# Kernel tuning notes

Hardware: AMD Instinct MI355X
Metric: run time of the kernel (lower is better)

## Reference

```python
import jax, jax.numpy as jnp
import numpy as np
from jax import lax

B, T, I, H, L = 256, 512, 156, 128, 32


def setup_inputs() -> dict:
    key = jax.random.key(0)
    ks = jax.random.split(key, 16)
    kb = 1.0 / np.sqrt(H)  # torch default LSTM/Linear init bound

    def u(k, shape, bound):
        return jax.random.uniform(k, shape, minval=-bound, maxval=bound, dtype=jnp.float32)

    return {
        "motion": jax.random.normal(ks[0], (B, T, I), dtype=jnp.float32),
        "eps": jax.random.normal(ks[1], (B, L), dtype=jnp.float32),
        # encoder LSTM (gate order i,f,g,o; b = b_ih + b_hh folded together)
        "enc_Wih": u(ks[2], (4 * H, I), kb),
        "enc_Whh": u(ks[3], (4 * H, H), kb),
        "enc_b": u(ks[4], (4 * H,), kb),
        "mu_W": u(ks[5], (L, H), kb),
        "mu_b": u(ks[6], (L,), kb),
        "var_W": u(ks[7], (L, H), kb),
        "var_b": u(ks[8], (L,), kb),
        # decoder
        "dec_fc_W": u(ks[9], (H, L), 1.0 / np.sqrt(L)),
        "dec_fc_b": u(ks[10], (H,), 1.0 / np.sqrt(L)),
        "dec_Wih": u(ks[11], (4 * H, H), kb),
        "dec_Whh": u(ks[12], (4 * H, H), kb),
        "dec_b": u(ks[13], (4 * H,), kb),
        "out_W": u(ks[14], (I, H), kb),
        "out_b": u(ks[15], (I,), kb),
    }


def _cell(gates, c):
    # PyTorch LSTM gate layout: [i, f, g, o] along the 4H axis
    i, f, g, o = jnp.split(gates, 4, axis=-1)
    c_new = jax.nn.sigmoid(f) * c + jax.nn.sigmoid(i) * jnp.tanh(g)
    h_new = jax.nn.sigmoid(o) * jnp.tanh(c_new)
    return h_new, c_new


def reference(motion, eps, enc_Wih, enc_Whh, enc_b, mu_W, mu_b, var_W, var_b,
              dec_fc_W, dec_fc_b, dec_Wih, dec_Whh, dec_b, out_W, out_b):
    b, t, _ = motion.shape

    # ---- encoder LSTM: single scan over time, keep only final hidden ----
    def enc_step(carry, x_t):
        h, c = carry
        gates = x_t @ enc_Wih.T + h @ enc_Whh.T + enc_b
        h, c = _cell(gates, c)
        return (h, c), None

    h0 = jnp.zeros((b, H), motion.dtype)
    c0 = jnp.zeros((b, H), motion.dtype)
    (h_fin, _), _ = lax.scan(enc_step, (h0, c0), jnp.swapaxes(motion, 0, 1))

    mu = h_fin @ mu_W.T + mu_b          # [B, L]
    logvar = h_fin @ var_W.T + var_b    # [B, L] ('var' in the torch code)

    # ---- reparameterize ----
    z = mu + eps * jnp.exp(0.5 * logvar)

    # ---- decoder: input at each step is the previous hidden state ----
    dh0 = z @ dec_fc_W.T + dec_fc_b     # [B, H]
    dc0 = jnp.zeros((b, H), motion.dtype)

    def dec_step(carry, _):
        h, c = carry
        gates = h @ dec_Wih.T + h @ dec_Whh.T + dec_b
        h, c = _cell(gates, c)
        return (h, c), h

    _, hs = lax.scan(dec_step, (dh0, dc0), None, length=t)  # [T, B, H]
    recon = jnp.einsum('tbh,oh->bto', hs, out_W) + out_b    # [B, T, I]

    # ---- losses ----
    rec_loss = jnp.mean((recon - motion) ** 2)
    kl_loss = -0.5 * jnp.sum(1.0 + logvar - mu ** 2 - jnp.exp(logvar))
    total = rec_loss + kl_loss
    return recon, mu, logvar, total
```

## Files before the change

### kernel.cpp

```cpp
#include <hip/hip_runtime.h>
#include <hip/hip_fp16.h>

#define B_ 256
#define T_ 512
#define I_ 156
#define H_ 128
#define L_ 32
#define G_ 512

typedef _Float16 half_t;
typedef _Float16 h2_t __attribute__((ext_vector_type(2)));

union U8 { uint4 u; h2_t h2[4]; };

__device__ __forceinline__ float fdot2(h2_t a, h2_t b, float c) {
#if __has_builtin(__builtin_amdgcn_fdot2)
  return __builtin_amdgcn_fdot2(a, b, c, false);
#else
  return c + (float)a[0] * (float)b[0] + (float)a[1] * (float)b[1];
#endif
}

__device__ __forceinline__ h2_t pk2(float a, float b) {
  h2_t r; r[0] = (half_t)a; r[1] = (half_t)b; return r;
}

__device__ __forceinline__ float sigf(float x) { return 1.0f / (1.0f + __expf(-x)); }
__device__ __forceinline__ float tanhf_(float x) {
  x = fminf(fmaxf(x, -20.f), 20.f);
  float e = __expf(2.f * x);
  return (e - 1.f) / (e + 1.f);
}

__global__ __launch_bounds__(1024, 4) void enc_kernel(
    const float* __restrict__ motion, const float* __restrict__ eps,
    const float* __restrict__ Wih, const float* __restrict__ Whh,
    const float* __restrict__ bv,
    const float* __restrict__ muW, const float* __restrict__ mub,
    const float* __restrict__ varW, const float* __restrict__ varb,
    const float* __restrict__ fcW, const float* __restrict__ fcb,
    float* __restrict__ dout, float* __restrict__ dh0,
    float* __restrict__ accums)
{
  const int tid  = threadIdx.x;
  const int part = tid >> 9;
  const int j    = tid & 511;
  const int b    = blockIdx.x;

  __shared__ h2_t xs[2][80];
  __shared__ h2_t hs[64];
  __shared__ float gl2[2][G_];
  __shared__ float hf[H_];
  __shared__ float mulv[64];
  __shared__ float zs[L_];

  h2_t wih[40];
  h2_t whh[32];
  {
    const int cbase = part * 80;
    const float* wr = Wih + (size_t)j * I_;
#pragma unroll
    for (int k = 0; k < 40; ++k) {
      int c0 = cbase + 2 * k;
      float a = (c0     < I_) ? wr[c0]     : 0.f;
      float c = (c0 + 1 < I_) ? wr[c0 + 1] : 0.f;
      wih[k] = pk2(a, c);
    }
    const float2* r2 = (const float2*)(Whh + (size_t)j * H_ + part * 64);
#pragma unroll
    for (int k = 0; k < 32; ++k) { float2 w = r2[k]; whh[k] = pk2(w.x, w.y); }
  }

  float cb0 = 0.f, cb1 = 0.f, cb2 = 0.f, cb3 = 0.f;
  if (tid < H_) {
    cb0 = bv[tid]; cb1 = bv[tid + H_]; cb2 = bv[tid + 2*H_]; cb3 = bv[tid + 3*H_];
  }

  float creg = 0.f, hreg = 0.f;
  if (tid < 64) hs[tid] = pk2(0.f, 0.f);
  if (tid < 4)  xs[tid >> 1][78 + (tid & 1)] = pk2(0.f, 0.f);

  const float2* mrow = (const float2*)(motion + (size_t)b * T_ * I_);
  const bool loader = (part == 1) && (j < 78);
  if (loader) { float2 m = mrow[j]; xs[0][j] = pk2(m.x, m.y); }
  __syncthreads();

  int cur = 0;
  float2 xreg;
  for (int t = 0; t < T_; ++t) {
    if (loader && t + 1 < T_) xreg = mrow[(t + 1) * 78 + j];

    float a0 = 0.f, a1 = 0.f, a2 = 0.f, a3 = 0.f;
    const U8* xv = (const U8*)&xs[cur][part * 40];
#pragma unroll
    for (int c = 0; c < 10; ++c) {
      U8 v = xv[c];
      a0 = fdot2(wih[4*c+0], v.h2[0], a0);
      a1 = fdot2(wih[4*c+1], v.h2[1], a1);
      a2 = fdot2(wih[4*c+2], v.h2[2], a2);
      a3 = fdot2(wih[4*c+3], v.h2[3], a3);
    }
    const U8* hv = (const U8*)&hs[part * 32];
#pragma unroll
    for (int c = 0; c < 8; ++c) {
      U8 v = hv[c];
      a0 = fdot2(whh[4*c+0], v.h2[0], a0);
      a1 = fdot2(whh[4*c+1], v.h2[1], a1);
      a2 = fdot2(whh[4*c+2], v.h2[2], a2);
      a3 = fdot2(whh[4*c+3], v.h2[3], a3);
    }
    gl2[part][j] = (a0 + a1) + (a2 + a3);
    if (loader && t + 1 < T_) xs[cur ^ 1][j] = pk2(xreg.x, xreg.y);
    __syncthreads();

    if (tid < H_) {
      float ig = gl2[0][tid]         + gl2[1][tid]         + cb0;
      float fg = gl2[0][tid +   H_]  + gl2[1][tid +   H_]  + cb1;
      float gg = gl2[0][tid + 2*H_]  + gl2[1][tid + 2*H_]  + cb2;
      float og = gl2[0][tid + 3*H_]  + gl2[1][tid + 3*H_]  + cb3;
      creg = sigf(fg) * creg + sigf(ig) * tanhf_(gg);
      hreg = sigf(og) * tanhf_(creg);
      ((half_t*)hs)[tid] = (half_t)hreg;
    }
    __syncthreads();
    cur ^= 1;
  }

  if (tid < H_) hf[tid] = hreg;
  __syncthreads();

  if (tid < 64) {
    const float* wr = (tid < L_) ? (muW + tid * H_) : (varW + (tid - L_) * H_);
    float a = (tid < L_) ? mub[tid] : varb[tid - L_];
#pragma unroll 8
    for (int k = 0; k < H_; ++k) a += wr[k] * hf[k];
    mulv[tid] = a;
    if (tid < L_) dout[(size_t)B_*T_*I_ + b * L_ + tid] = a;
    else          dout[(size_t)B_*T_*I_ + B_*L_ + b * L_ + (tid - L_)] = a;
  }
  __syncthreads();

  if (tid < L_) {
    float mu = mulv[tid], lv = mulv[tid + L_];
    float z = mu + eps[b * L_ + tid] * __expf(0.5f * lv);
    zs[tid] = z;
    float kt = 1.f + lv - mu * mu - __expf(lv);
#pragma unroll
    for (int off = 16; off > 0; off >>= 1) kt += __shfl_down(kt, off, 64);
    if (tid == 0) atomicAdd(&accums[1], kt);
  }
  __syncthreads();

  if (tid < H_) {
    const float* wr = fcW + tid * L_;
    float a = fcb[tid];
#pragma unroll
    for (int l = 0; l < L_; ++l) a += wr[l] * zs[l];
    dh0[b * H_ + tid] = a;
  }
}

__global__ __launch_bounds__(1024, 4) void dec_kernel(
    const float* __restrict__ motion,
    const float* __restrict__ Wih, const float* __restrict__ Whh,
    const float* __restrict__ bv,
    const float* __restrict__ oW, const float* __restrict__ ob,
    const float* __restrict__ dh0,
    float* __restrict__ dout, float* __restrict__ accums)
{
  const int tid  = threadIdx.x;
  const int part = tid >> 9;
  const int j    = tid & 511;
  const int b    = blockIdx.x;

  __shared__ h2_t hs[64];
  __shared__ float gl[G_];
  __shared__ float red[16];

  h2_t wv[64];
  float bj = 0.f;
  if (part == 0) {
    const float2* r1 = (const float2*)(Wih + (size_t)j * H_);
    const float2* r2 = (const float2*)(Whh + (size_t)j * H_);
#pragma unroll
    for (int k = 0; k < 64; ++k) {
      float2 a = r1[k], c = r2[k];
      wv[k] = pk2(a.x + c.x, a.y + c.y);
    }
    bj = bv[j];
  } else if (j < I_) {
    const float2* r = (const float2*)(oW + (size_t)j * H_);
#pragma unroll
    for (int k = 0; k < 64; ++k) { float2 w = r[k]; wv[k] = pk2(w.x, w.y); }
    bj = ob[j];
  }

  float creg = 0.f, hreg = 0.f;
  if (tid < H_) {
    hreg = dh0[b * H_ + tid];
    ((half_t*)hs)[tid] = (half_t)hreg;
  }
  __syncthreads();

  const float* mr = motion + (size_t)b * T_ * I_;
  float* rr = dout + (size_t)b * T_ * I_;
  float rl = 0.f;

  for (int t = 0; t < T_; ++t) {
    if (part == 0) {
      float a0 = 0.f, a1 = 0.f, a2 = 0.f, a3 = 0.f;
      const U8* hv = (const U8*)hs;
#pragma unroll
      for (int c = 0; c < 16; ++c) {
        U8 v = hv[c];
        a0 = fdot2(wv[4*c+0], v.h2[0], a0);
        a1 = fdot2(wv[4*c+1], v.h2[1], a1);
        a2 = fdot2(wv[4*c+2], v.h2[2], a2);
        a3 = fdot2(wv[4*c+3], v.h2[3], a3);
      }
      gl[j] = bj + (a0 + a1) + (a2 + a3);
    } else if (j < I_ && t > 0) {
      float a0 = 0.f, a1 = 0.f, a2 = 0.f, a3 = 0.f;
      const U8* hv = (const U8*)hs;
#pragma unroll
      for (int c = 0; c < 16; ++c) {
        U8 v = hv[c];
        a0 = fdot2(wv[4*c+0], v.h2[0], a0);
        a1 = fdot2(wv[4*c+1], v.h2[1], a1);
        a2 = fdot2(wv[4*c+2], v.h2[2], a2);
        a3 = fdot2(wv[4*c+3], v.h2[3], a3);
      }
      float r = bj + (a0 + a1) + (a2 + a3);
      rr[(t - 1) * I_ + j] = r;
      float d = r - mr[(t - 1) * I_ + j];
      rl += d * d;
    }
    __syncthreads();

    if (tid < H_) {
      float ig = gl[tid], fg = gl[tid + H_], gg = gl[tid + 2*H_], og = gl[tid + 3*H_];
      creg = sigf(fg) * creg + sigf(ig) * tanhf_(gg);
      hreg = sigf(og) * tanhf_(creg);
      ((half_t*)hs)[tid] = (half_t)hreg;
    }
    __syncthreads();
  }

  if (part == 1 && j < I_) {
    float a0 = 0.f, a1 = 0.f, a2 = 0.f, a3 = 0.f;
    const U8* hv = (const U8*)hs;
#pragma unroll
    for (int c = 0; c < 16; ++c) {
      U8 v = hv[c];
      a0 = fdot2(wv[4*c+0], v.h2[0], a0);
      a1 = fdot2(wv[4*c+1], v.h2[1], a1);
      a2 = fdot2(wv[4*c+2], v.h2[2], a2);
      a3 = fdot2(wv[4*c+3], v.h2[3], a3);
    }
    float r = bj + (a0 + a1) + (a2 + a3);
    rr[511 * I_ + j] = r;
    float d = r - mr[511 * I_ + j];
    rl += d * d;
  }

  float v = rl;
#pragma unroll
  for (int off = 32; off > 0; off >>= 1) v += __shfl_down(v, off, 64);
  if ((tid & 63) == 0) red[tid >> 6] = v;
  __syncthreads();
  if (tid == 0) {
    float s = 0.f;
#pragma unroll
    for (int w = 0; w < 16; ++w) s += red[w];
    atomicAdd(&accums[0], s);
  }
}

__global__ void init_kernel(float* accums) {
  if (threadIdx.x < 2) accums[threadIdx.x] = 0.f;
}

__global__ void fin_kernel(const float* __restrict__ accums, float* __restrict__ dout) {
  if (threadIdx.x == 0) {
    float rec = accums[0] / (float)((size_t)B_ * T_ * I_);
    float kl = -0.5f * accums[1];
    dout[(size_t)B_*T_*I_ + 2 * B_ * L_] = rec + kl;
  }
}

extern "C" void kernel_launch(void* const* d_in, const int* in_sizes, int n_in,
                              void* d_out, int out_size, void* d_ws, size_t ws_size,
                              hipStream_t stream) {
  const float* motion = (const float*)d_in[0];
  const float* eps    = (const float*)d_in[1];
  const float* eWih   = (const float*)d_in[2];
  const float* eWhh   = (const float*)d_in[3];
  const float* eb     = (const float*)d_in[4];
  const float* muW    = (const float*)d_in[5];
  const float* mub    = (const float*)d_in[6];
  const float* varW   = (const float*)d_in[7];
  const float* varb   = (const float*)d_in[8];
  const float* fcW    = (const float*)d_in[9];
  const float* fcb    = (const float*)d_in[10];
  const float* dWih   = (const float*)d_in[11];
  const float* dWhh   = (const float*)d_in[12];
  const float* db     = (const float*)d_in[13];
  const float* oW     = (const float*)d_in[14];
  const float* obv    = (const float*)d_in[15];
  float* out = (float*)d_out;
  float* accums = (float*)d_ws;
  float* dh0    = (float*)d_ws + 16;

  hipLaunchKernelGGL(init_kernel, dim3(1), dim3(64), 0, stream, accums);
  hipLaunchKernelGGL(enc_kernel, dim3(B_), dim3(1024), 0, stream,
                     motion, eps, eWih, eWhh, eb, muW, mub, varW, varb, fcW, fcb,
                     out, dh0, accums);
  hipLaunchKernelGGL(dec_kernel, dim3(B_), dim3(1024), 0, stream,
                     motion, dWih, dWhh, db, oW, obv, dh0, out, accums);
  hipLaunchKernelGGL(fin_kernel, dim3(1), dim3(64), 0, stream, accums, out);
}
```

Measured before the change: 1.162 ms.

## Precompute encoder input projection in a parallel kernel and split decoder work

Adds a separate highly parallel kernel that computes the encoder input projection x_t·Wih^T + b for all timesteps into an fp16 workspace buffer. The recurrent encoder kernel then reads one precomputed value per gate instead of doing the input matmul inside the serial time loop. The decoder is also restructured: all 1024 threads now split the gate dot products in halves, the output projection is split four ways across threads, and partial sums are reduced one step later through double-buffered shared memory. The trade-off is a large extra workspace write and read of about 128 MB, plus an fp16 rounding of the projected inputs. It falls back to the old encoder when the workspace is too small.

```diff
diff --git a/kernel.cpp b/kernel.cpp
--- a/kernel.cpp
+++ b/kernel.cpp
@@ -32,7 +32,180 @@
   return (e - 1.f) / (e + 1.f);
 }
 
-__global__ __launch_bounds__(1024, 4) void enc_kernel(
+__global__ __launch_bounds__(1024) void xproj_kernel(
+    const float* __restrict__ motion, const float* __restrict__ Wih,
+    const float* __restrict__ bv, half_t* __restrict__ XP)
+{
+  const int tid = threadIdx.x;
+  const int kpart = tid >> 9;
+  const int j = tid & 511;
+
+  __shared__ h2_t xb[8][80];
+  __shared__ float pp[8][512][2];
+
+  h2_t wih[40];
+  {
+    const float* wr = Wih + (size_t)j * I_;
+#pragma unroll
+    for (int k = 0; k < 40; ++k) {
+      int c0 = kpart * 80 + 2 * k;
+      float a = (c0     < I_) ? wr[c0]     : 0.f;
+      float c = (c0 + 1 < I_) ? wr[c0 + 1] : 0.f;
+      wih[k] = pk2(a, c);
+    }
+  }
+  const float bj = (kpart == 0) ? bv[j] : 0.f;
+
+  const float2* mf2 = (const float2*)motion;
+  const int blk = blockIdx.x;
+
+  for (int c = 0; c < 8; ++c) {
+    const int rowbase = blk * 64 + c * 8;
+    if (tid < 624) {
+      int r = tid / 78, e = tid % 78;
+      float2 m = mf2[(size_t)(rowbase + r) * 78 + e];
+      xb[r][e] = pk2(m.x, m.y);
+    } else if (tid < 640) {
+      int r = tid - 624;
+      xb[r][78] = pk2(0.f, 0.f); xb[r][79] = pk2(0.f, 0.f);
+    }
+    __syncthreads();
+#pragma unroll
+    for (int r = 0; r < 8; ++r) {
+      float a0 = bj, a1 = 0.f;
+      const U8* xv = (const U8*)&xb[r][kpart * 40];
+#pragma unroll
+      for (int q = 0; q < 5; ++q) {
+        U8 v0 = xv[2*q], v1 = xv[2*q+1];
+        a0 = fdot2(wih[8*q+0], v0.h2[0], a0);
+        a1 = fdot2(wih[8*q+1], v0.h2[1], a1);
+        a0 = fdot2(wih[8*q+2], v0.h2[2], a0);
+        a1 = fdot2(wih[8*q+3], v0.h2[3], a1);
+        a0 = fdot2(wih[8*q+4], v1.h2[0], a0);
+        a1 = fdot2(wih[8*q+5], v1.h2[1], a1);
+        a0 = fdot2(wih[8*q+6], v1.h2[2], a0);
+        a1 = fdot2(wih[8*q+7], v1.h2[3], a1);
+      }
+      pp[r][j][kpart] = a0 + a1;
+    }
+    __syncthreads();
+#pragma unroll
+    for (int k = 0; k < 4; ++k) {
+      int idx = tid + k * 1024;
+      int r = idx >> 9, jj = idx & 511;
+      XP[(size_t)(rowbase + r) * 512 + jj] = (half_t)(pp[r][jj][0] + pp[r][jj][1]);
+    }
+    __syncthreads();
+  }
+}
+
+__global__ __launch_bounds__(1024) void enc_rec_kernel(
+    const half_t* __restrict__ XP, const float* __restrict__ eps,
+    const float* __restrict__ Whh,
+    const float* __restrict__ muW, const float* __restrict__ mub,
+    const float* __restrict__ varW, const float* __restrict__ varb,
+    const float* __restrict__ fcW, const float* __restrict__ fcb,
+    float* __restrict__ dout, float* __restrict__ dh0,
+    float* __restrict__ accums)
+{
+  const int tid  = threadIdx.x;
+  const int part = tid >> 9;
+  const int j    = tid & 511;
+  const int b    = blockIdx.x;
+
+  __shared__ h2_t hs[64];
+  __shared__ float gl2[2][G_];
+  __shared__ float hf[H_];
+  __shared__ float mulv[64];
+  __shared__ float zs[L_];
+
+  h2_t whh[32];
+  {
+    const float2* r2 = (const float2*)Whh;
+#pragma unroll
+    for (int k = 0; k < 32; ++k) {
+      float2 w = r2[(size_t)j * 64 + part * 32 + k];
+      whh[k] = pk2(w.x, w.y);
+    }
+  }
+
+  float creg = 0.f, hreg = 0.f;
+  if (tid < 64) hs[tid] = pk2(0.f, 0.f);
+  __syncthreads();
+
+  const half_t* xpb = XP + (size_t)b * 512 * 512 + j;
+  half_t xpc = (half_t)0.f, xpn = (half_t)0.f;
+  if (part == 0) xpc = xpb[0];
+
+  for (int t = 0; t < T_; ++t) {
+    if (part == 0 && t + 1 < T_) xpn = xpb[(size_t)(t + 1) * 512];
+
+    float a0 = (part == 0) ? (float)xpc : 0.f;
+    float a1 = 0.f;
+    const U8* hv = (const U8*)&hs[part * 32];
+#pragma unroll
+    for (int q = 0; q < 4; ++q) {
+      U8 v0 = hv[2*q], v1 = hv[2*q+1];
+      a0 = fdot2(whh[8*q+0], v0.h2[0], a0);
+      a1 = fdot2(whh[8*q+1], v0.h2[1], a1);
+      a0 = fdot2(whh[8*q+2], v0.h2[2], a0);
+      a1 = fdot2(whh[8*q+3], v0.h2[3], a1);
+      a0 = fdot2(whh[8*q+4], v1.h2[0], a0);
+      a1 = fdot2(whh[8*q+5], v1.h2[1], a1);
+      a0 = fdot2(whh[8*q+6], v1.h2[2], a0);
+      a1 = fdot2(whh[8*q+7], v1.h2[3], a1);
+    }
+    gl2[part][j] = a0 + a1;
+    __syncthreads();
+
+    if (tid < H_) {
+      float ig = gl2[0][tid]        + gl2[1][tid];
+      float fg = gl2[0][tid +   H_] + gl2[1][tid +   H_];
+      float gg = gl2[0][tid + 2*H_] + gl2[1][tid + 2*H_];
+      float og = gl2[0][tid + 3*H_] + gl2[1][tid + 3*H_];
+      creg = sigf(fg) * creg + sigf(ig) * tanhf_(gg);
+      hreg = sigf(og) * tanhf_(creg);
+      ((half_t*)hs)[tid] = (half_t)hreg;
+    }
+    __syncthreads();
+    xpc = xpn;
+  }
+
+  if (tid < H_) hf[tid] = hreg;
+  __syncthreads();
+
+  if (tid < 64) {
+    const float* wr = (tid < L_) ? (muW + tid * H_) : (varW + (tid - L_) * H_);
+    float a = (tid < L_) ? mub[tid] : varb[tid - L_];
+#pragma unroll 8
+    for (int k = 0; k < H_; ++k) a += wr[k] * hf[k];
+    mulv[tid] = a;
+    if (tid < L_) dout[(size_t)B_*T_*I_ + b * L_ + tid] = a;
+    else          dout[(size_t)B_*T_*I_ + B_*L_ + b * L_ + (tid - L_)] = a;
+  }
+  __syncthreads();
+
+  if (tid < L_) {
+    float mu = mulv[tid], lv = mulv[tid + L_];
+    float z = mu + eps[b * L_ + tid] * __expf(0.5f * lv);
+    zs[tid] = z;
+    float kt = 1.f + lv - mu * mu - __expf(lv);
+#pragma unroll
+    for (int off = 16; off > 0; off >>= 1) kt += __shfl_down(kt, off, 64);
+    if (tid == 0) atomicAdd(&accums[1], kt);
+  }
+  __syncthreads();
+
+  if (tid < H_) {
+    const float* wr = fcW + tid * L_;
+    float a = fcb[tid];
+#pragma unroll
+    for (int l = 0; l < L_; ++l) a += wr[l] * zs[l];
+    dh0[b * H_ + tid] = a;
+  }
+}
+
+__global__ __launch_bounds__(1024) void enc_fb_kernel(
     const float* __restrict__ motion, const float* __restrict__ eps,
     const float* __restrict__ Wih, const float* __restrict__ Whh,
     const float* __restrict__ bv,
@@ -114,10 +287,10 @@
     __syncthreads();
 
     if (tid < H_) {
-      float ig = gl2[0][tid]         + gl2[1][tid]         + cb0;
-      float fg = gl2[0][tid +   H_]  + gl2[1][tid +   H_]  + cb1;
-      float gg = gl2[0][tid + 2*H_]  + gl2[1][tid + 2*H_]  + cb2;
-      float og = gl2[0][tid + 3*H_]  + gl2[1][tid + 3*H_]  + cb3;
+      float ig = gl2[0][tid]        + gl2[1][tid]        + cb0;
+      float fg = gl2[0][tid +   H_] + gl2[1][tid +   H_] + cb1;
+      float gg = gl2[0][tid + 2*H_] + gl2[1][tid + 2*H_] + cb2;
+      float og = gl2[0][tid + 3*H_] + gl2[1][tid + 3*H_] + cb3;
       creg = sigf(fg) * creg + sigf(ig) * tanhf_(gg);
       hreg = sigf(og) * tanhf_(creg);
       ((half_t*)hs)[tid] = (half_t)hreg;
@@ -160,7 +333,7 @@
   }
 }
 
-__global__ __launch_bounds__(1024, 4) void dec_kernel(
+__global__ __launch_bounds__(1024) void dec_kernel(
     const float* __restrict__ motion,
     const float* __restrict__ Wih, const float* __restrict__ Whh,
     const float* __restrict__ bv,
@@ -174,26 +347,39 @@
   const int b    = blockIdx.x;
 
   __shared__ h2_t hs[64];
-  __shared__ float gl[G_];
+  __shared__ float gl2[2][G_];
+  __shared__ float pp[2][156][4];
   __shared__ float red[16];
 
-  h2_t wv[64];
-  float bj = 0.f;
-  if (part == 0) {
-    const float2* r1 = (const float2*)(Wih + (size_t)j * H_);
-    const float2* r2 = (const float2*)(Whh + (size_t)j * H_);
-#pragma unroll
-    for (int k = 0; k < 64; ++k) {
-      float2 a = r1[k], c = r2[k];
-      wv[k] = pk2(a.x + c.x, a.y + c.y);
-    }
-    bj = bv[j];
-  } else if (j < I_) {
-    const float2* r = (const float2*)(oW + (size_t)j * H_);
-#pragma unroll
-    for (int k = 0; k < 64; ++k) { float2 w = r[k]; wv[k] = pk2(w.x, w.y); }
-    bj = ob[j];
-  }
+  h2_t wd[32];
+  {
+    const float2* r1 = (const float2*)Wih;
+    const float2* r2 = (const float2*)Whh;
+#pragma unroll
+    for (int k = 0; k < 32; ++k) {
+      float2 a = r1[(size_t)j * 64 + part * 32 + k];
+      float2 c = r2[(size_t)j * 64 + part * 32 + k];
+      wd[k] = pk2(a.x + c.x, a.y + c.y);
+    }
+  }
+  const float breg = (part == 0) ? bv[j] : 0.f;
+
+  const bool isproj = tid < 624;
+  const int pcol = isproj ? (tid % 156) : 0;
+  const int pk   = isproj ? (tid / 156) : 0;
+  h2_t wo[16];
+  float obreg = 0.f;
+  if (isproj) {
+    const float2* r = (const float2*)oW;
+#pragma unroll
+    for (int k = 0; k < 16; ++k) {
+      float2 w = r[(size_t)pcol * 64 + pk * 16 + k];
+      wo[k] = pk2(w.x, w.y);
+    }
+    if (pk == 0) obreg = ob[pcol];
+  }
+  const bool isfin = (tid >= 624) && (tid < 780);
+  const int fcol = isfin ? (tid - 624) : 0;
 
   float creg = 0.f, hreg = 0.f;
   if (tid < H_) {
@@ -207,38 +393,50 @@
   float rl = 0.f;
 
   for (int t = 0; t < T_; ++t) {
-    if (part == 0) {
-      float a0 = 0.f, a1 = 0.f, a2 = 0.f, a3 = 0.f;
-      const U8* hv = (const U8*)hs;
-#pragma unroll
-      for (int c = 0; c < 16; ++c) {
-        U8 v = hv[c];
-        a0 = fdot2(wv[4*c+0], v.h2[0], a0);
-        a1 = fdot2(wv[4*c+1], v.h2[1], a1);
-        a2 = fdot2(wv[4*c+2], v.h2[2], a2);
-        a3 = fdot2(wv[4*c+3], v.h2[3], a3);
+    {
+      float a0 = breg, a1 = 0.f;
+      const U8* hv = (const U8*)&hs[part * 32];
+#pragma unroll
+      for (int q = 0; q < 4; ++q) {
+        U8 v0 = hv[2*q], v1 = hv[2*q+1];
+        a0 = fdot2(wd[8*q+0], v0.h2[0], a0);
+        a1 = fdot2(wd[8*q+1], v0.h2[1], a1);
+        a0 = fdot2(wd[8*q+2], v0.h2[2], a0);
+        a1 = fdot2(wd[8*q+3], v0.h2[3], a1);
+        a0 = fdot2(wd[8*q+4], v1.h2[0], a0);
+        a1 = fdot2(wd[8*q+5], v1.h2[1], a1);
+        a0 = fdot2(wd[8*q+6], v1.h2[2], a0);
+        a1 = fdot2(wd[8*q+7], v1.h2[3], a1);
       }
-      gl[j] = bj + (a0 + a1) + (a2 + a3);
-    } else if (j < I_ && t > 0) {
-      float a0 = 0.f, a1 = 0.f, a2 = 0.f, a3 = 0.f;
-      const U8* hv = (const U8*)hs;
-#pragma unroll
-      for (int c = 0; c < 16; ++c) {
-        U8 v = hv[c];
-        a0 = fdot2(wv[4*c+0], v.h2[0], a0);
-        a1 = fdot2(wv[4*c+1], v.h2[1], a1);
-        a2 = fdot2(wv[4*c+2], v.h2[2], a2);
-        a3 = fdot2(wv[4*c+3], v.h2[3], a3);
+      gl2[part][j] = a0 + a1;
+    }
+    if (isproj) {
+      float pa = obreg;
+      const U8* hv = (const U8*)&hs[pk * 16];
+#pragma unroll
+      for (int q = 0; q < 4; ++q) {
+        U8 v = hv[q];
+        pa = fdot2(wo[4*q+0], v.h2[0], pa);
+        pa = fdot2(wo[4*q+1], v.h2[1], pa);
+        pa = fdot2(wo[4*q+2], v.h2[2], pa);
+        pa = fdot2(wo[4*q+3], v.h2[3], pa);
       }
-      float r = bj + (a0 + a1) + (a2 + a3);
-      rr[(t - 1) * I_ + j] = r;
-      float d = r - mr[(t - 1) * I_ + j];
+      pp[t & 1][pcol][pk] = pa;
+    }
+    if (isfin && t >= 2) {
+      int par = (t - 1) & 1;
+      float v = pp[par][fcol][0] + pp[par][fcol][1] + pp[par][fcol][2] + pp[par][fcol][3];
+      rr[(size_t)(t - 2) * I_ + fcol] = v;
+      float d = v - mr[(size_t)(t - 2) * I_ + fcol];
       rl += d * d;
     }
     __syncthreads();
 
     if (tid < H_) {
-      float ig = gl[tid], fg = gl[tid + H_], gg = gl[tid + 2*H_], og = gl[tid + 3*H_];
+      float ig = gl2[0][tid]        + gl2[1][tid];
+      float fg = gl2[0][tid +   H_] + gl2[1][tid +   H_];
+      float gg = gl2[0][tid + 2*H_] + gl2[1][tid + 2*H_];
+      float og = gl2[0][tid + 3*H_] + gl2[1][tid + 3*H_];
       creg = sigf(fg) * creg + sigf(ig) * tanhf_(gg);
       hreg = sigf(og) * tanhf_(creg);
       ((half_t*)hs)[tid] = (half_t)hreg;
@@ -246,20 +444,30 @@
     __syncthreads();
   }
 
-  if (part == 1 && j < I_) {
-    float a0 = 0.f, a1 = 0.f, a2 = 0.f, a3 = 0.f;
-    const U8* hv = (const U8*)hs;
-#pragma unroll
-    for (int c = 0; c < 16; ++c) {
-      U8 v = hv[c];
-      a0 = fdot2(wv[4*c+0], v.h2[0], a0);
-      a1 = fdot2(wv[4*c+1], v.h2[1], a1);
-      a2 = fdot2(wv[4*c+2], v.h2[2], a2);
-      a3 = fdot2(wv[4*c+3], v.h2[3], a3);
-    }
-    float r = bj + (a0 + a1) + (a2 + a3);
-    rr[511 * I_ + j] = r;
-    float d = r - mr[511 * I_ + j];
+  if (isproj) {
+    float pa = obreg;
+    const U8* hv = (const U8*)&hs[pk * 16];
+#pragma unroll
+    for (int q = 0; q < 4; ++q) {
+      U8 v = hv[q];
+      pa = fdot2(wo[4*q+0], v.h2[0], pa);
+      pa = fdot2(wo[4*q+1], v.h2[1], pa);
+      pa = fdot2(wo[4*q+2], v.h2[2], pa);
+      pa = fdot2(wo[4*q+3], v.h2[3], pa);
+    }
+    pp[0][pcol][pk] = pa;
+  }
+  if (isfin) {
+    float v = pp[1][fcol][0] + pp[1][fcol][1] + pp[1][fcol][2] + pp[1][fcol][3];
+    rr[(size_t)510 * I_ + fcol] = v;
+    float d = v - mr[(size_t)510 * I_ + fcol];
+    rl += d * d;
+  }
+  __syncthreads();
+  if (isfin) {
+    float v = pp[0][fcol][0] + pp[0][fcol][1] + pp[0][fcol][2] + pp[0][fcol][3];
+    rr[(size_t)511 * I_ + fcol] = v;
+    float d = v - mr[(size_t)511 * I_ + fcol];
     rl += d * d;
   }
 
@@ -308,13 +516,26 @@
   const float* oW     = (const float*)d_in[14];
   const float* obv    = (const float*)d_in[15];
   float* out = (float*)d_out;
+
   float* accums = (float*)d_ws;
-  float* dh0    = (float*)d_ws + 16;
+  float* dh0    = (float*)((char*)d_ws + 256);
+  const size_t xp_off = 256 + 131072;
+  const size_t need = xp_off + (size_t)B_ * T_ * 512 * sizeof(half_t);
+  const bool big = ws_size >= need;
+  half_t* XP = (half_t*)((char*)d_ws + xp_off);
 
   hipLaunchKernelGGL(init_kernel, dim3(1), dim3(64), 0, stream, accums);
-  hipLaunchKernelGGL(enc_kernel, dim3(B_), dim3(1024), 0, stream,
-                     motion, eps, eWih, eWhh, eb, muW, mub, varW, varb, fcW, fcb,
-                     out, dh0, accums);
+  if (big) {
+    hipLaunchKernelGGL(xproj_kernel, dim3(2048), dim3(1024), 0, stream,
+                       motion, eWih, eb, XP);
+    hipLaunchKernelGGL(enc_rec_kernel, dim3(B_), dim3(1024), 0, stream,
+                       XP, eps, eWhh, muW, mub, varW, varb, fcW, fcb,
+                       out, dh0, accums);
+  } else {
+    hipLaunchKernelGGL(enc_fb_kernel, dim3(B_), dim3(1024), 0, stream,
+                       motion, eps, eWih, eWhh, eb, muW, mub, varW, varb, fcW, fcb,
+                       out, dh0, accums);
+  }
   hipLaunchKernelGGL(dec_kernel, dim3(B_), dim3(1024), 0, stream,
                      motion, dWih, dWhh, db, oW, obv, dh0, out, accums);
   hipLaunchKernelGGL(fin_kernel, dim3(1), dim3(64), 0, stream, accums, out);
```

Result: slower. 1.406 ms (+21.0%).
